# Kernel optimization log

Hardware: AMD Instinct MI355X
Metric: run time of the kernel (lower is better)

The kernel has to match this reference:

```python
import jax, jax.numpy as jnp
import numpy as np

B, T, D, E, K = 4, 4096, 2048, 64, 2


def setup_inputs() -> dict:
    key = jax.random.key(0)
    k1, k2 = jax.random.split(key)
    x = jax.random.normal(k1, (B, T, D), dtype=jnp.float32)
    # nn.Linear(token_dim, n_experts, bias=False) weight: [E, D]
    gate_w = jax.random.normal(k2, (E, D), dtype=jnp.float32) * (1.0 / np.sqrt(D))
    return {"x": x, "gate_w": gate_w}


def reference(x, gate_w):
    # logits = x @ gate_w.T : [B, T, E]
    logits = jnp.einsum("btd,ed->bte", x, gate_w)
    scores, indices = jax.lax.top_k(logits, K)  # [B, T, K] each
    weights = jax.nn.softmax(scores, axis=-1)
    return weights, indices
```

## Files before the change

kernel.cpp:

```cpp
#include <hip/hip_runtime.h>
#include <math.h>


#define NTOK 16384
#define DDIM 2048
#define NEXP 64
#define TBLK 128
#define KC   32
#define NS   4
#define SLICE_ELTS (NTOK * NEXP)

typedef __attribute__((ext_vector_type(8))) _Float16 f16x8;
typedef __attribute__((ext_vector_type(4))) float f32x4;

__device__ static inline void gload_lds16(const void* gsrc, void* ldst) {
    __builtin_amdgcn_global_load_lds(
        (const __attribute__((address_space(1))) void*)gsrc,
        (__attribute__((address_space(3))) void*)ldst, 16, 0, 0);
}

__device__ static inline void split2h(float x, _Float16& h, _Float16& m) {
    h = (_Float16)x;
    float r = x - (float)h;
    m = (_Float16)r;
}

__global__ __launch_bounds__(256) void wsplit_kernel(
    const float* __restrict__ gw, _Float16* __restrict__ wh,
    _Float16* __restrict__ wm)
{
    for (int i = blockIdx.x * 256 + threadIdx.x; i < NEXP * DDIM;
         i += gridDim.x * 256) {
        _Float16 h, m;
        split2h(gw[i], h, m);
        wh[i] = h; wm[i] = m;
    }
}

__global__ __launch_bounds__(256, 2) void moe_mfma_kernel(
    const float* __restrict__ x,
    const _Float16* __restrict__ wh,
    const _Float16* __restrict__ wm,
    float* __restrict__ part)
{
    __shared__ float4 XF[3][TBLK * 8];
    __shared__ f16x8  WH[2][NEXP * 4], WM[2][NEXP * 4];

    const int tid  = threadIdx.x;
    const int lane = tid & 63;
    const int w    = tid >> 6;
    const int dsl  = blockIdx.x & (NS - 1);
    const int tg   = blockIdx.x / NS;
    const int T0   = tg * TBLK;
    const int KSL  = DDIM / NS;
    const int NCH  = KSL / KC;
    const int k0s  = dsl * KSL;

    const int we  = tid >> 2;
    const int wsk = ((tid & 3) ^ ((we >> 1) & 3)) * 8;

    const int fr  = lane & 15;
    const int fg  = lane >> 4;
    const int fsw = fg ^ ((fr >> 1) & 3);
    const int akey = fr & 7;

    f32x4 acc[2][4];
#pragma unroll
    for (int mi = 0; mi < 2; ++mi)
#pragma unroll
        for (int n = 0; n < 4; ++n) acc[mi][n] = (f32x4){0.f, 0.f, 0.f, 0.f};

#define XSTAGE(ch, buf)                                                       \
    {                                                                         \
        const int kk = k0s + (ch) * KC;                                       \
        _Pragma("unroll")                                                     \
        for (int s = 0; s < 4; ++s) {                                         \
            const int u   = tid + s * 256;                                    \
            const int tok = u >> 3;                                           \
            const int c   = (u & 7) ^ (tok & 7);                              \
            gload_lds16(x + (size_t)(T0 + tok) * DDIM + kk + c * 4,           \
                        &XF[buf][u]);                                         \
        }                                                                     \
    }
#define WSTAGE(ch, buf)                                                       \
    {                                                                         \
        const size_t woff = (size_t)we * DDIM + k0s + (ch) * KC + wsk;        \
        gload_lds16(wh + woff, &WH[buf][tid]);                                \
        gload_lds16(wm + woff, &WM[buf][tid]);                                \
    }
#define WAIT4 asm volatile("s_waitcnt vmcnt(4)" ::: "memory")
#define WAIT0 asm volatile("s_waitcnt vmcnt(0)" ::: "memory")
#define BAR   __builtin_amdgcn_s_barrier()

    XSTAGE(0, 0); WSTAGE(0, 0); XSTAGE(1, 1);
    WAIT4; BAR;

    for (int ch = 0; ch < NCH; ++ch) {
        const int xb = ch % 3;
        const int wb = ch & 1;
        if (ch + 1 < NCH) WSTAGE(ch + 1, (ch + 1) & 1);
        if (ch + 2 < NCH) XSTAGE(ch + 2, (ch + 2) % 3);

        const float4* Xc = XF[xb];
        f16x8 ah[2], am[2];
#pragma unroll
        for (int mi = 0; mi < 2; ++mi) {
            const int arow = (w * 32 + mi * 16 + fr) * 8;
            float4 a0 = Xc[arow + ((fg * 2 + 0) ^ akey)];
            float4 a1 = Xc[arow + ((fg * 2 + 1) ^ akey)];
            float xf8[8] = {a0.x, a0.y, a0.z, a0.w, a1.x, a1.y, a1.z, a1.w};
#pragma unroll
            for (int j = 0; j < 8; ++j) {
                _Float16 hj, mj;
                split2h(xf8[j], hj, mj);
                ah[mi][j] = hj; am[mi][j] = mj;
            }
        }

#pragma unroll
        for (int n = 0; n < 4; ++n) {
            const int bidx = (n * 16 + fr) * 4 + fsw;
            const f16x8 bh = WH[wb][bidx];
            const f16x8 bm = WM[wb][bidx];
#pragma unroll
            for (int mi = 0; mi < 2; ++mi) {
                acc[mi][n] = __builtin_amdgcn_mfma_f32_16x16x32_f16(am[mi], bm, acc[mi][n], 0, 0, 0);
                acc[mi][n] = __builtin_amdgcn_mfma_f32_16x16x32_f16(am[mi], bh, acc[mi][n], 0, 0, 0);
                acc[mi][n] = __builtin_amdgcn_mfma_f32_16x16x32_f16(ah[mi], bm, acc[mi][n], 0, 0, 0);
                acc[mi][n] = __builtin_amdgcn_mfma_f32_16x16x32_f16(ah[mi], bh, acc[mi][n], 0, 0, 0);
            }
        }

        if (ch + 2 < NCH)      { WAIT4; BAR; }
        else if (ch + 1 < NCH) { WAIT0; BAR; }
    }
#undef XSTAGE
#undef WSTAGE
#undef WAIT4
#undef WAIT0
#undef BAR

    float* wsl = part + (size_t)dsl * SLICE_ELTS;
#pragma unroll
    for (int mi = 0; mi < 2; ++mi)
#pragma unroll
        for (int n = 0; n < 4; ++n)
#pragma unroll
            for (int j = 0; j < 4; ++j) {
                const int tok = T0 + w * 32 + mi * 16 + fg * 4 + j;
                wsl[(size_t)tok * NEXP + n * 16 + fr] = acc[mi][n][j];
            }
}

__global__ __launch_bounds__(128) void moe_reduce_kernel(
    const float* __restrict__ part,
    float* __restrict__ out)
{
    const int t = blockIdx.x * 128 + threadIdx.x;
    float m1 = -INFINITY, m2 = -INFINITY;
    int i1 = 0, i2 = 0;

    const float* base = part + (size_t)t * NEXP;
    for (int e4 = 0; e4 < 16; ++e4) {
        float4 s = *reinterpret_cast<const float4*>(base + e4 * 4);
#pragma unroll
        for (int sl = 1; sl < NS; ++sl) {
            float4 p = *reinterpret_cast<const float4*>(
                base + (size_t)sl * SLICE_ELTS + e4 * 4);
            s.x += p.x; s.y += p.y; s.z += p.z; s.w += p.w;
        }
        float v[4] = {s.x, s.y, s.z, s.w};
#pragma unroll
        for (int q = 0; q < 4; ++q) {
            const int e = e4 * 4 + q;
            if (v[q] > m1) {
                m2 = m1; i2 = i1;
                m1 = v[q]; i1 = e;
            } else if (v[q] > m2) {
                m2 = v[q]; i2 = e;
            }
        }
    }

    float e2 = expf(m2 - m1);
    float denom = 1.f + e2;
    out[t * 2 + 0] = 1.f / denom;
    out[t * 2 + 1] = e2 / denom;
    out[NTOK * 2 + t * 2 + 0] = (float)i1;
    out[NTOK * 2 + t * 2 + 1] = (float)i2;
}

extern "C" void kernel_launch(void* const* d_in, const int* in_sizes, int n_in,
                              void* d_out, int out_size, void* d_ws, size_t ws_size,
                              hipStream_t stream) {
    const float* x  = (const float*)d_in[0];
    const float* gw = (const float*)d_in[1];
    float* out = (float*)d_out;

    _Float16* wh = (_Float16*)d_ws;
    _Float16* wm = wh + NEXP * DDIM;
    float* part = (float*)((char*)d_ws + (1 << 20));

    wsplit_kernel<<<dim3(128), dim3(256), 0, stream>>>(gw, wh, wm);
    moe_mfma_kernel<<<dim3((NTOK / TBLK) * NS), dim3(256), 0, stream>>>(
        x, wh, wm, part);
    moe_reduce_kernel<<<dim3(NTOK / 128), dim3(128), 0, stream>>>(part, out);
}
```

Before: 47.59 us.

## Fuse split-K reduction and top-2 softmax into the MFMA GEMM kernel

Replaces the across-block split-K and separate reduce kernel with one block of 8 waves per 64-token tile. The four K-groups are split across wave pairs inside the block, and their partial logits are summed through LDS. Top-2 and softmax then run in the same kernel. This removes the global partial-logit buffer write and read-back plus one launch. The cost is 160 KB of dynamic LDS, which allows only one block per CU, and a grid of exactly 256 blocks.

```diff
diff --git a/kernel.cpp b/kernel.cpp
--- a/kernel.cpp
+++ b/kernel.cpp
@@ -5,13 +5,18 @@
 #define NTOK 16384
 #define DDIM 2048
 #define NEXP 64
-#define TBLK 128
+#define TBLK 64
 #define KC   32
-#define NS   4
-#define SLICE_ELTS (NTOK * NEXP)
+#define NKG  4
+#define KSL  (DDIM / NKG)
+#define NCH  (KSL / KC)
 
 typedef __attribute__((ext_vector_type(8))) _Float16 f16x8;
 typedef __attribute__((ext_vector_type(4))) float f32x4;
+
+#define XF_OFF 0
+#define WH_OFF 98304
+#define WM_OFF 131072
 
 __device__ static inline void gload_lds16(const void* gsrc, void* ldst) {
     __builtin_amdgcn_global_load_lds(
@@ -37,27 +42,24 @@
     }
 }
 
-__global__ __launch_bounds__(256, 2) void moe_mfma_kernel(
+__global__ __launch_bounds__(512, 1) void moe_fused_kernel(
     const float* __restrict__ x,
     const _Float16* __restrict__ wh,
     const _Float16* __restrict__ wm,
-    float* __restrict__ part)
+    float* __restrict__ out)
 {
-    __shared__ float4 XF[3][TBLK * 8];
-    __shared__ f16x8  WH[2][NEXP * 4], WM[2][NEXP * 4];
+    extern __shared__ char smem[];
+    float4* XF = (float4*)(smem + XF_OFF);
+    f16x8*  WH = (f16x8*)(smem + WH_OFF);
+    f16x8*  WM = (f16x8*)(smem + WM_OFF);
+    float*  red = (float*)smem;
 
     const int tid  = threadIdx.x;
     const int lane = tid & 63;
     const int w    = tid >> 6;
-    const int dsl  = blockIdx.x & (NS - 1);
-    const int tg   = blockIdx.x / NS;
-    const int T0   = tg * TBLK;
-    const int KSL  = DDIM / NS;
-    const int NCH  = KSL / KC;
-    const int k0s  = dsl * KSL;
-
-    const int we  = tid >> 2;
-    const int wsk = ((tid & 3) ^ ((we >> 1) & 3)) * 8;
+    const int kg   = w >> 1;
+    const int tq   = w & 1;
+    const int T0   = blockIdx.x * TBLK;
 
     const int fr  = lane & 15;
     const int fg  = lane >> 4;
@@ -72,21 +74,28 @@
 
 #define XSTAGE(ch, buf)                                                       \
     {                                                                         \
-        const int kk = k0s + (ch) * KC;                                       \
         _Pragma("unroll")                                                     \
-        for (int s = 0; s < 4; ++s) {                                         \
-            const int u   = tid + s * 256;                                    \
-            const int tok = u >> 3;                                           \
-            const int c   = (u & 7) ^ (tok & 7);                              \
-            gload_lds16(x + (size_t)(T0 + tok) * DDIM + kk + c * 4,           \
-                        &XF[buf][u]);                                         \
+        for (int k = 0; k < 4; ++k) {                                         \
+            const int u = tid + k * 512;                                      \
+            const int s = u >> 9;                                             \
+            const int r = (u >> 3) & 63;                                      \
+            const int c = (u & 7) ^ (r & 7);                                  \
+            gload_lds16(x + (size_t)(T0 + r) * DDIM + s * KSL + (ch) * KC + c * 4, \
+                        &XF[(buf) * 2048 + u]);                               \
         }                                                                     \
     }
 #define WSTAGE(ch, buf)                                                       \
     {                                                                         \
-        const size_t woff = (size_t)we * DDIM + k0s + (ch) * KC + wsk;        \
-        gload_lds16(wh + woff, &WH[buf][tid]);                                \
-        gload_lds16(wm + woff, &WM[buf][tid]);                                \
+        _Pragma("unroll")                                                     \
+        for (int k = 0; k < 2; ++k) {                                         \
+            const int v = tid + k * 512;                                      \
+            const int s = v >> 8;                                             \
+            const int e = (v >> 2) & 63;                                      \
+            const int c = (v & 3) ^ ((e >> 1) & 3);                           \
+            const size_t off = (size_t)e * DDIM + s * KSL + (ch) * KC + c * 8;\
+            gload_lds16(wh + off, &WH[(buf) * 1024 + v]);                     \
+            gload_lds16(wm + off, &WM[(buf) * 1024 + v]);                     \
+        }                                                                     \
     }
 #define WAIT4 asm volatile("s_waitcnt vmcnt(4)" ::: "memory")
 #define WAIT0 asm volatile("s_waitcnt vmcnt(0)" ::: "memory")
@@ -101,11 +110,11 @@
         if (ch + 1 < NCH) WSTAGE(ch + 1, (ch + 1) & 1);
         if (ch + 2 < NCH) XSTAGE(ch + 2, (ch + 2) % 3);
 
-        const float4* Xc = XF[xb];
+        const float4* Xc = &XF[xb * 2048 + kg * 512];
         f16x8 ah[2], am[2];
 #pragma unroll
         for (int mi = 0; mi < 2; ++mi) {
-            const int arow = (w * 32 + mi * 16 + fr) * 8;
+            const int arow = (tq * 32 + mi * 16 + fr) * 8;
             float4 a0 = Xc[arow + ((fg * 2 + 0) ^ akey)];
             float4 a1 = Xc[arow + ((fg * 2 + 1) ^ akey)];
             float xf8[8] = {a0.x, a0.y, a0.z, a0.w, a1.x, a1.y, a1.z, a1.w};
@@ -117,11 +126,13 @@
             }
         }
 
+        const f16x8* WHc = &WH[wb * 1024 + kg * 256];
+        const f16x8* WMc = &WM[wb * 1024 + kg * 256];
 #pragma unroll
         for (int n = 0; n < 4; ++n) {
             const int bidx = (n * 16 + fr) * 4 + fsw;
-            const f16x8 bh = WH[wb][bidx];
-            const f16x8 bm = WM[wb][bidx];
+            const f16x8 bh = WHc[bidx];
+            const f16x8 bm = WMc[bidx];
 #pragma unroll
             for (int mi = 0; mi < 2; ++mi) {
                 acc[mi][n] = __builtin_amdgcn_mfma_f32_16x16x32_f16(am[mi], bm, acc[mi][n], 0, 0, 0);
@@ -133,6 +144,7 @@
 
         if (ch + 2 < NCH)      { WAIT4; BAR; }
         else if (ch + 1 < NCH) { WAIT0; BAR; }
+        else                   { BAR; }
     }
 #undef XSTAGE
 #undef WSTAGE
@@ -140,54 +152,52 @@
 #undef WAIT0
 #undef BAR
 
-    float* wsl = part + (size_t)dsl * SLICE_ELTS;
 #pragma unroll
     for (int mi = 0; mi < 2; ++mi)
 #pragma unroll
         for (int n = 0; n < 4; ++n)
 #pragma unroll
             for (int j = 0; j < 4; ++j) {
-                const int tok = T0 + w * 32 + mi * 16 + fg * 4 + j;
-                wsl[(size_t)tok * NEXP + n * 16 + fr] = acc[mi][n][j];
-            }
-}
-
-__global__ __launch_bounds__(128) void moe_reduce_kernel(
-    const float* __restrict__ part,
-    float* __restrict__ out)
-{
-    const int t = blockIdx.x * 128 + threadIdx.x;
-    float m1 = -INFINITY, m2 = -INFINITY;
-    int i1 = 0, i2 = 0;
-
-    const float* base = part + (size_t)t * NEXP;
-    for (int e4 = 0; e4 < 16; ++e4) {
-        float4 s = *reinterpret_cast<const float4*>(base + e4 * 4);
-#pragma unroll
-        for (int sl = 1; sl < NS; ++sl) {
-            float4 p = *reinterpret_cast<const float4*>(
-                base + (size_t)sl * SLICE_ELTS + e4 * 4);
-            s.x += p.x; s.y += p.y; s.z += p.z; s.w += p.w;
+                const int e = n * 16 + fr;
+                const int t = tq * 32 + mi * 16 + fg * 4 + j;
+                red[kg * 4160 + e * 65 + t] = acc[mi][n][j];
+            }
+    __syncthreads();
+
+#pragma unroll
+    for (int k = 0; k < 8; ++k) {
+        const int q = tid + k * 512;
+        const int e = q >> 6;
+        const int t = q & 63;
+        float s = red[0 * 4160 + e * 65 + t];
+#pragma unroll
+        for (int sl = 1; sl < NKG; ++sl)
+            s += red[sl * 4160 + e * 65 + t];
+        red[e * 65 + t] = s;
+    }
+    __syncthreads();
+
+    if (tid < TBLK) {
+        const int t = tid;
+        float m1 = -INFINITY, m2 = -INFINITY;
+        int i1 = 0, i2 = 0;
+        for (int e = 0; e < NEXP; ++e) {
+            float v = red[e * 65 + t];
+            if (v > m1) {
+                m2 = m1; i2 = i1;
+                m1 = v;  i1 = e;
+            } else if (v > m2) {
+                m2 = v;  i2 = e;
+            }
         }
-        float v[4] = {s.x, s.y, s.z, s.w};
-#pragma unroll
-        for (int q = 0; q < 4; ++q) {
-            const int e = e4 * 4 + q;
-            if (v[q] > m1) {
-                m2 = m1; i2 = i1;
-                m1 = v[q]; i1 = e;
-            } else if (v[q] > m2) {
-                m2 = v[q]; i2 = e;
-            }
-        }
-    }
-
-    float e2 = expf(m2 - m1);
-    float denom = 1.f + e2;
-    out[t * 2 + 0] = 1.f / denom;
-    out[t * 2 + 1] = e2 / denom;
-    out[NTOK * 2 + t * 2 + 0] = (float)i1;
-    out[NTOK * 2 + t * 2 + 1] = (float)i2;
+        float e2 = expf(m2 - m1);
+        float denom = 1.f + e2;
+        const int gt = T0 + t;
+        out[gt * 2 + 0] = 1.f / denom;
+        out[gt * 2 + 1] = e2 / denom;
+        out[NTOK * 2 + gt * 2 + 0] = (float)i1;
+        out[NTOK * 2 + gt * 2 + 1] = (float)i2;
+    }
 }
 
 extern "C" void kernel_launch(void* const* d_in, const int* in_sizes, int n_in,
@@ -199,10 +209,8 @@
 
     _Float16* wh = (_Float16*)d_ws;
     _Float16* wm = wh + NEXP * DDIM;
-    float* part = (float*)((char*)d_ws + (1 << 20));
 
     wsplit_kernel<<<dim3(128), dim3(256), 0, stream>>>(gw, wh, wm);
-    moe_mfma_kernel<<<dim3((NTOK / TBLK) * NS), dim3(256), 0, stream>>>(
-        x, wh, wm, part);
-    moe_reduce_kernel<<<dim3(NTOK / 128), dim3(128), 0, stream>>>(part, out);
-}
+    moe_fused_kernel<<<dim3(NTOK / TBLK), dim3(512), 163840, stream>>>(
+        x, wh, wm, out);
+}
```

Measured after the change: 44.63 us. 1.07x faster.
